# Optimization experiments

Measured on AMD Instinct MI355X. Metric: run time of the kernel, lower is better.

## Reference

```python
import jax, jax.numpy as jnp
import numpy as np

NUM_HEAD = 16


def setup_inputs() -> dict:
    key = jax.random.key(0)
    k1, k2, k3 = jax.random.split(key, 3)
    E = 1024
    x = jax.random.normal(k1, (4, 2048, E), dtype=jnp.float32)
    W1 = jax.random.normal(k2, (E, 3 * E), dtype=jnp.float32) * 0.02
    b1 = jnp.zeros((3 * E,), dtype=jnp.float32)
    W2 = jax.random.normal(k3, (E, E), dtype=jnp.float32) * 0.02
    b2 = jnp.zeros((E,), dtype=jnp.float32)
    return {"x": x, "W1": W1, "b1": b1, "W2": W2, "b2": b2}


def reference(x, W1, b1, W2, b2):
    # Fused QKV projection: (n, s, 3E)
    h = x @ W1 + b1
    n, s, _ = h.shape
    # Split into heads FIRST (matches torch reshape), then transpose: (n, H, s, 3*d_head)
    h = h.reshape(n, s, NUM_HEAD, -1).transpose(0, 2, 1, 3)
    # Chunk last dim into q, k, v: each (n, H, s, d_head)
    q, k, v = jnp.split(h, 3, axis=-1)
    dk = jnp.asarray(v.shape[-1], x.dtype) ** 0.5
    # Naive full S x S attention (faithful to source)
    w = jnp.einsum("nhqd,nhkd->nhqk", q, k) / dk
    w = jax.nn.softmax(w, axis=-1)  # dropout1 is identity at eval
    att = jnp.einsum("nhqk,nhkd->nhqd", w, v)
    att = att.transpose(0, 2, 1, 3).reshape(n, s, -1)  # (n, s, E)
    return att @ W2 + b2  # dropout2 identity at eval
```

## Files before the change

### kernel.cpp

```cpp
#include <hip/hip_runtime.h>
#include <math.h>
#include <stdint.h>
#include <stddef.h>


#define SEQ    2048
#define NB     4
#define E_DIM  1024
#define N1     3072
#define M_TOK  8192
#define NHEAD  16
#define DHEAD  64

typedef __attribute__((ext_vector_type(4))) float    floatx4;
typedef __attribute__((ext_vector_type(8))) short    shortx8;
typedef __attribute__((ext_vector_type(4))) short    shortx4;
typedef __attribute__((ext_vector_type(4))) unsigned short ushortx4;

#if __has_builtin(__builtin_amdgcn_exp2f)
#define EXP2(x) __builtin_amdgcn_exp2f(x)
#else
#define EXP2(x) __expf((x) * 0.6931471805599453f)
#endif

#define MFMA_K16(a, b, c) \
    __builtin_amdgcn_mfma_f32_16x16x16bf16_1k((a), (b), (c), 0, 0, 0)

__device__ __forceinline__ unsigned short f2bf(float f) {
    union { float f; unsigned u; } v; v.f = f;
    unsigned r = (v.u + 0x7FFFu + ((v.u >> 16) & 1u)) >> 16;
    return (unsigned short)r;
}
__device__ __forceinline__ unsigned fbits(float f) {
    union { float f; unsigned u; } v; v.f = f; return v.u;
}
__device__ __forceinline__ float bitsf(unsigned u) {
    union { unsigned u; float f; } v; v.u = u; return v.f;
}

__device__ __forceinline__ void gl_lds16(const void* g, void* l) {
    __builtin_amdgcn_global_load_lds(
        (const __attribute__((address_space(1))) unsigned int*)g,
        (__attribute__((address_space(3))) unsigned int*)l, 16, 0, 0);
}

__global__ __launch_bounds__(256) void cvt_bf16(
    const float* __restrict__ in, unsigned short* __restrict__ out)
{
    const size_t i = ((size_t)blockIdx.x * 256 + threadIdx.x) * 8;
    float4 a = *(const float4*)(in + i);
    float4 b = *(const float4*)(in + i + 4);
    ushortx4 o0 = { f2bf(a.x), f2bf(a.y), f2bf(a.z), f2bf(a.w) };
    ushortx4 o1 = { f2bf(b.x), f2bf(b.y), f2bf(b.z), f2bf(b.w) };
    *(ushortx4*)(out + i)     = o0;
    *(ushortx4*)(out + i + 4) = o1;
}

__global__ __launch_bounds__(256) void cvt_transpose(
    const float* __restrict__ W, unsigned short* __restrict__ Wt, int K, int N)
{
    __shared__ unsigned short tile[32][33];
    const int tx = threadIdx.x, ty = threadIdx.y;
    const int n0 = blockIdx.x * 32, k0 = blockIdx.y * 32;
#pragma unroll
    for (int r = 0; r < 4; ++r) {
        const int k = ty + r * 8;
        tile[tx][k] = f2bf(W[(size_t)(k0 + k) * N + n0 + tx]);
    }
    __syncthreads();
#pragma unroll
    for (int r = 0; r < 4; ++r) {
        const int n = ty + r * 8;
        Wt[(size_t)(n0 + n) * K + k0 + tx] = tile[n][tx];
    }
}

template <bool OUT_BF16, bool FUSE>
__global__ __launch_bounds__(256) void gemm_bf16(
    const short* __restrict__ A, const short* __restrict__ Bt,
    const float* __restrict__ bias, void* __restrict__ Cout,
    unsigned short* __restrict__ Vt,
    int M, int N, int K)
{
    __shared__ short As[2][128 * 64];
    __shared__ short Bs[2][128 * 64];

    const int t    = threadIdx.x;
    const int lane = t & 63, w = t >> 6;
    const int quad = lane >> 4, l15 = lane & 15;
    const int bm = blockIdx.y * 128, bn = blockIdx.x * 128;
    const int m0w = (w >> 1) * 64, n0w = (w & 1) * 64;

    const int srow   = t >> 3;
    const int schunk = t & 7;
    const int gch    = schunk ^ (srow & 7);
    const short* Ag = A  + (size_t)(bm + srow) * K + gch * 8;
    const short* Bg = Bt + (size_t)(bn + srow) * K + gch * 8;
    const int sOff = srow * 64 + schunk * 8;

    floatx4 acc[4][4];
#pragma unroll
    for (int i = 0; i < 4; ++i)
#pragma unroll
        for (int j = 0; j < 4; ++j) acc[i][j] = (floatx4)0.f;

    const int NK = K >> 6;

#define GEMM_STAGE(bufi, k0)                                                   \
    {                                                                          \
        _Pragma("unroll")                                                      \
        for (int r = 0; r < 4; ++r) {                                          \
            gl_lds16(Ag + (size_t)(r * 32) * K + (k0), &As[bufi][sOff + r * 32 * 64]); \
            gl_lds16(Bg + (size_t)(r * 32) * K + (k0), &Bs[bufi][sOff + r * 32 * 64]); \
        }                                                                      \
    }

    GEMM_STAGE(0, 0);
    GEMM_STAGE(1, 64);

    for (int kt = 0; kt < NK; ++kt) {
        const int buf = kt & 1;
        if (kt + 1 < NK) asm volatile("s_waitcnt vmcnt(8)" ::: "memory");
        else             asm volatile("s_waitcnt vmcnt(0)" ::: "memory");
        __builtin_amdgcn_sched_barrier(0);
        __builtin_amdgcn_s_barrier();
        __builtin_amdgcn_sched_barrier(0);

#pragma unroll
        for (int kk = 0; kk < 2; ++kk) {
            shortx8 af[4], bf[4];
#pragma unroll
            for (int mi = 0; mi < 4; ++mi)
                af[mi] = *(const shortx8*)(&As[buf][(m0w + mi * 16 + l15) * 64
                                           + (((kk * 4 + quad) ^ (l15 & 7)) * 8)]);
#pragma unroll
            for (int ni = 0; ni < 4; ++ni)
                bf[ni] = *(const shortx8*)(&Bs[buf][(n0w + ni * 16 + l15) * 64
                                           + (((kk * 4 + quad) ^ (l15 & 7)) * 8)]);
#pragma unroll
            for (int mi = 0; mi < 4; ++mi)
#pragma unroll
                for (int ni = 0; ni < 4; ++ni)
                    acc[mi][ni] = __builtin_amdgcn_mfma_f32_16x16x32_bf16(
                        af[mi], bf[ni], acc[mi][ni], 0, 0, 0);
        }

        __builtin_amdgcn_sched_barrier(0);
        __builtin_amdgcn_s_barrier();
        __builtin_amdgcn_sched_barrier(0);
        if (kt + 2 < NK) GEMM_STAGE(buf, (kt + 2) * 64);
    }
#undef GEMM_STAGE

    float bv[4];
#pragma unroll
    for (int ni = 0; ni < 4; ++ni) bv[ni] = bias[bn + n0w + ni * 16 + l15];

#pragma unroll
    for (int ni = 0; ni < 4; ++ni) {
        const int col   = bn + n0w + ni * 16 + l15;
        const int cm    = col % 192;
        const int vhead = col / 192;
#pragma unroll
        for (int mi = 0; mi < 4; ++mi) {
            const int row0 = bm + m0w + mi * 16 + quad * 4;
            float v[4];
#pragma unroll
            for (int r = 0; r < 4; ++r) v[r] = acc[mi][ni][r] + bv[ni];
            if (OUT_BF16) {
                if (FUSE && cm < DHEAD) {
#pragma unroll
                    for (int r = 0; r < 4; ++r) v[r] *= 0.18033688011112042f;
                }
                unsigned short* H = (unsigned short*)Cout;
#pragma unroll
                for (int r = 0; r < 4; ++r)
                    H[(size_t)(row0 + r) * N + col] = f2bf(v[r]);
                if (FUSE && cm >= 2 * DHEAD) {
                    const int nb = row0 >> 11;
                    const int s  = row0 & 2047;
                    const int d  = cm - 2 * DHEAD;
                    ushortx4 pk = { f2bf(v[0]), f2bf(v[1]), f2bf(v[2]), f2bf(v[3]) };
                    *(ushortx4*)(Vt + ((size_t)(nb * NHEAD + vhead) * DHEAD + d) * SEQ + s) = pk;
                }
            } else {
                float* C = (float*)Cout;
#pragma unroll
                for (int r = 0; r < 4; ++r)
                    C[(size_t)(row0 + r) * N + col] = v[r];
            }
        }
    }
}

__global__ __launch_bounds__(256, 4) void attn_mfma(
    const short* __restrict__ h, const short* __restrict__ Vt,
    unsigned short* __restrict__ att)
{
    __shared__ short Ks[2][64 * 64];
    __shared__ short Vs[2][64 * 64];

    const int t    = threadIdx.x;
    const int lane = t & 63, w = t >> 6;
    const int quad = lane >> 4, l15 = lane & 15;
    const int r7   = l15 & 7;
    const int bh = blockIdx.x, n = bh >> 4, head = bh & 15;
    const int q0 = blockIdx.y * 128 + w * 32;

    const short* hQ  = h + (size_t)n * SEQ * N1 + head * (3 * DHEAD);
    const short* hK  = hQ + DHEAD;
    const short* Vtb = Vt + (size_t)bh * DHEAD * SEQ;

    const int srow = t >> 2;
    const int sc0  = (t & 3) * 2;
    const int sk   = srow & 7;
    const short* gK = hK  + (size_t)srow * N1  + sc0 * 8;
    const short* gV = Vtb + (size_t)srow * SEQ + sc0 * 8;
    const int oL0 = srow * 64 + ((sc0    ) ^ sk) * 8;
    const int oL1 = srow * 64 + ((sc0 + 1) ^ sk) * 8;

    shortx8 qf[2][2];
#pragma unroll
    for (int qt = 0; qt < 2; ++qt)
#pragma unroll
        for (int kt = 0; kt < 2; ++kt)
            qf[qt][kt] = *(const shortx8*)(hQ + (size_t)(q0 + qt * 16 + l15) * N1
                                           + kt * 32 + quad * 8);

    floatx4 O[2][4];
    floatx4 Osum[2];
#pragma unroll
    for (int qt = 0; qt < 2; ++qt) {
        Osum[qt] = (floatx4)0.f;
#pragma unroll
        for (int dt = 0; dt < 4; ++dt) O[qt][dt] = (floatx4)0.f;
    }

    const shortx4 ones = { (short)0x3F80, (short)0x3F80, (short)0x3F80, (short)0x3F80 };

    const int NT = SEQ / 64;

    int4 ka = *(const int4*)gK, kb = *(const int4*)(gK + 8);
    int4 va = *(const int4*)gV, vb = *(const int4*)(gV + 8);
    *(int4*)(&Ks[0][oL0]) = ka; *(int4*)(&Ks[0][oL1]) = kb;
    *(int4*)(&Vs[0][oL0]) = va; *(int4*)(&Vs[0][oL1]) = vb;
    gK += (size_t)64 * N1; gV += 64;

    for (int it = 0; it < NT; ++it) {
        const int buf = it & 1;
        __syncthreads();

        const bool more = (it + 1 < NT);
        if (more) {
            ka = *(const int4*)gK; kb = *(const int4*)(gK + 8);
            va = *(const int4*)gV; vb = *(const int4*)(gV + 8);
            gK += (size_t)64 * N1; gV += 64;
        }

        const short* Kb = &Ks[buf][0];
        const short* Vb = &Vs[buf][0];

#pragma unroll
        for (int sl = 0; sl < 4; ++sl) {
            const short* krow = Kb + (sl * 16 + l15) * 64;
            shortx8 kf0 = *(const shortx8*)(krow + ((quad ^ r7) * 8));
            shortx8 kf1 = *(const shortx8*)(krow + (((quad ^ 4) ^ r7) * 8));
            shortx4 vf[4];
#pragma unroll
            for (int dt = 0; dt < 4; ++dt)
                vf[dt] = *(const shortx4*)(Vb + (dt * 16 + l15) * 64
                                           + (((sl * 4 + quad) ^ (r7 << 1)) << 2));

            shortx4 pa[2];
#pragma unroll
            for (int qt = 0; qt < 2; ++qt) {
                floatx4 s = __builtin_amdgcn_mfma_f32_16x16x32_bf16(
                    kf0, qf[qt][0], (floatx4)0.f, 0, 0, 0);
                s = __builtin_amdgcn_mfma_f32_16x16x32_bf16(
                    kf1, qf[qt][1], s, 0, 0, 0);
                const float p0 = EXP2(s[0]);
                const float p1 = EXP2(s[1]);
                const float p2 = EXP2(s[2]);
                const float p3 = EXP2(s[3]);
                union { uint2 u; shortx4 v; } cv;
                cv.u.x = __builtin_amdgcn_perm(fbits(p1), fbits(p0), 0x07060302u);
                cv.u.y = __builtin_amdgcn_perm(fbits(p3), fbits(p2), 0x07060302u);
                pa[qt] = cv.v;
            }

#pragma unroll
            for (int qt = 0; qt < 2; ++qt) {
                Osum[qt] = MFMA_K16(pa[qt], ones, Osum[qt]);
#pragma unroll
                for (int dt = 0; dt < 4; ++dt)
                    O[qt][dt] = MFMA_K16(pa[qt], vf[dt], O[qt][dt]);
            }
        }

        if (more) {
            short* Kn = &Ks[buf ^ 1][0];
            short* Vn = &Vs[buf ^ 1][0];
            *(int4*)(Kn + oL0) = ka; *(int4*)(Kn + oL1) = kb;
            *(int4*)(Vn + oL0) = va; *(int4*)(Vn + oL1) = vb;
        }
    }

    const size_t obase = ((size_t)n * SEQ + q0) * E_DIM + head * DHEAD;
#pragma unroll
    for (int qt = 0; qt < 2; ++qt)
#pragma unroll
        for (int r = 0; r < 4; ++r) {
            const float inv = 1.f / Osum[qt][r];
            const size_t row = obase + (size_t)(qt * 16 + quad * 4 + r) * E_DIM;
#pragma unroll
            for (int dt = 0; dt < 4; ++dt)
                att[row + dt * 16 + l15] = f2bf(O[qt][dt][r] * inv);
        }
}

extern "C" void kernel_launch(void* const* d_in, const int* in_sizes, int n_in,
                              void* d_out, int out_size, void* d_ws, size_t ws_size,
                              hipStream_t stream)
{
    const float* x  = (const float*)d_in[0];
    const float* W1 = (const float*)d_in[1];
    const float* b1 = (const float*)d_in[2];
    const float* W2 = (const float*)d_in[3];
    const float* b2 = (const float*)d_in[4];
    float* out = (float*)d_out;

    char* ws = (char*)d_ws;
    unsigned short* x_bf  = (unsigned short*)(ws);
    unsigned short* W1t   = (unsigned short*)(ws + (16u << 20));
    unsigned short* W2t   = (unsigned short*)(ws + (22u << 20));
    unsigned short* h_bf  = (unsigned short*)(ws + (24u << 20));
    unsigned short* attb  = (unsigned short*)(ws + (72u << 20));
    unsigned short* Vtw   = (unsigned short*)(ws + (88u << 20));

    cvt_bf16<<<dim3((M_TOK * E_DIM) / (256 * 8)), 256, 0, stream>>>(x, x_bf);
    cvt_transpose<<<dim3(N1 / 32, E_DIM / 32), dim3(32, 8), 0, stream>>>(W1, W1t, E_DIM, N1);
    cvt_transpose<<<dim3(E_DIM / 32, E_DIM / 32), dim3(32, 8), 0, stream>>>(W2, W2t, E_DIM, E_DIM);

    gemm_bf16<true, true><<<dim3(N1 / 128, M_TOK / 128), 256, 0, stream>>>(
        (const short*)x_bf, (const short*)W1t, b1, h_bf, Vtw, M_TOK, N1, E_DIM);

    attn_mfma<<<dim3(NB * NHEAD, SEQ / 128), 256, 0, stream>>>(
        (const short*)h_bf, (const short*)Vtw, attb);

    gemm_bf16<false, false><<<dim3(E_DIM / 128, M_TOK / 128), 256, 0, stream>>>(
        (const short*)attb, (const short*)W2t, b2, out, nullptr, M_TOK, E_DIM, E_DIM);
}
```

Before: 266.2 us.

## Rewrite attention inner loop with 32x32x16 MFMA and permlane32 P repacking

Replaces the 16x16 MFMA tiling of the attention kernel with 32x32x16 bf16 MFMAs, computing S^T per 32-key subtile and feeding P to the PV product after a permlane32_swap repack instead of a register round-trip. The row-sum of P is now accumulated with scalar adds and a cross-half shuffle, replacing the extra MFMA against a ones vector. It also raises wave priority around the compute section with s_setprio. The intent is fewer MFMA issues and less LDS fragment traffic per tile, at the cost of a new lane mapping that must be correct and possibly higher register pressure.

```diff
diff --git a/kernel.cpp b/kernel.cpp
--- a/kernel.cpp
+++ b/kernel.cpp
@@ -12,10 +12,11 @@
 #define NHEAD  16
 #define DHEAD  64
 
-typedef __attribute__((ext_vector_type(4))) float    floatx4;
-typedef __attribute__((ext_vector_type(8))) short    shortx8;
-typedef __attribute__((ext_vector_type(4))) short    shortx4;
-typedef __attribute__((ext_vector_type(4))) unsigned short ushortx4;
+typedef __attribute__((ext_vector_type(4)))  float    floatx4;
+typedef __attribute__((ext_vector_type(16))) float    floatx16;
+typedef __attribute__((ext_vector_type(8)))  short    shortx8;
+typedef __attribute__((ext_vector_type(4)))  short    shortx4;
+typedef __attribute__((ext_vector_type(4)))  unsigned short ushortx4;
 
 #if __has_builtin(__builtin_amdgcn_exp2f)
 #define EXP2(x) __builtin_amdgcn_exp2f(x)
@@ -23,8 +24,8 @@
 #define EXP2(x) __expf((x) * 0.6931471805599453f)
 #endif
 
-#define MFMA_K16(a, b, c) \
-    __builtin_amdgcn_mfma_f32_16x16x16bf16_1k((a), (b), (c), 0, 0, 0)
+#define MFMA32(a, b, c) \
+    __builtin_amdgcn_mfma_f32_32x32x16_bf16((a), (b), (c), 0, 0, 0)
 
 __device__ __forceinline__ unsigned short f2bf(float f) {
     union { float f; unsigned u; } v; v.f = f;
@@ -33,9 +34,6 @@
 }
 __device__ __forceinline__ unsigned fbits(float f) {
     union { float f; unsigned u; } v; v.f = f; return v.u;
-}
-__device__ __forceinline__ float bitsf(unsigned u) {
-    union { unsigned u; float f; } v; v.u = u; return v.f;
 }
 
 __device__ __forceinline__ void gl_lds16(const void* g, void* l) {
@@ -202,10 +200,9 @@
 
     const int t    = threadIdx.x;
     const int lane = t & 63, w = t >> 6;
-    const int quad = lane >> 4, l15 = lane & 15;
-    const int r7   = l15 & 7;
+    const int l31  = lane & 31, hf = lane >> 5;
     const int bh = blockIdx.x, n = bh >> 4, head = bh & 15;
-    const int q0 = blockIdx.y * 128 + w * 32;
+    const int q0w = blockIdx.y * 128 + w * 32;
 
     const short* hQ  = h + (size_t)n * SEQ * N1 + head * (3 * DHEAD);
     const short* hK  = hQ + DHEAD;
@@ -219,24 +216,14 @@
     const int oL0 = srow * 64 + ((sc0    ) ^ sk) * 8;
     const int oL1 = srow * 64 + ((sc0 + 1) ^ sk) * 8;
 
-    shortx8 qf[2][2];
-#pragma unroll
-    for (int qt = 0; qt < 2; ++qt)
-#pragma unroll
-        for (int kt = 0; kt < 2; ++kt)
-            qf[qt][kt] = *(const shortx8*)(hQ + (size_t)(q0 + qt * 16 + l15) * N1
-                                           + kt * 32 + quad * 8);
-
-    floatx4 O[2][4];
-    floatx4 Osum[2];
-#pragma unroll
-    for (int qt = 0; qt < 2; ++qt) {
-        Osum[qt] = (floatx4)0.f;
-#pragma unroll
-        for (int dt = 0; dt < 4; ++dt) O[qt][dt] = (floatx4)0.f;
-    }
-
-    const shortx4 ones = { (short)0x3F80, (short)0x3F80, (short)0x3F80, (short)0x3F80 };
+    shortx8 qf[4];
+#pragma unroll
+    for (int c = 0; c < 4; ++c)
+        qf[c] = *(const shortx8*)(hQ + (size_t)(q0w + l31) * N1 + c * 16 + hf * 8);
+
+    floatx16 O0 = (floatx16)0.f;
+    floatx16 O1 = (floatx16)0.f;
+    float ls0 = 0.f, ls1 = 0.f;
 
     const int NT = SEQ / 64;
 
@@ -260,42 +247,49 @@
         const short* Kb = &Ks[buf][0];
         const short* Vb = &Vs[buf][0];
 
-#pragma unroll
-        for (int sl = 0; sl < 4; ++sl) {
-            const short* krow = Kb + (sl * 16 + l15) * 64;
-            shortx8 kf0 = *(const shortx8*)(krow + ((quad ^ r7) * 8));
-            shortx8 kf1 = *(const shortx8*)(krow + (((quad ^ 4) ^ r7) * 8));
-            shortx4 vf[4];
-#pragma unroll
-            for (int dt = 0; dt < 4; ++dt)
-                vf[dt] = *(const shortx4*)(Vb + (dt * 16 + l15) * 64
-                                           + (((sl * 4 + quad) ^ (r7 << 1)) << 2));
-
-            shortx4 pa[2];
-#pragma unroll
-            for (int qt = 0; qt < 2; ++qt) {
-                floatx4 s = __builtin_amdgcn_mfma_f32_16x16x32_bf16(
-                    kf0, qf[qt][0], (floatx4)0.f, 0, 0, 0);
-                s = __builtin_amdgcn_mfma_f32_16x16x32_bf16(
-                    kf1, qf[qt][1], s, 0, 0, 0);
-                const float p0 = EXP2(s[0]);
-                const float p1 = EXP2(s[1]);
-                const float p2 = EXP2(s[2]);
-                const float p3 = EXP2(s[3]);
-                union { uint2 u; shortx4 v; } cv;
-                cv.u.x = __builtin_amdgcn_perm(fbits(p1), fbits(p0), 0x07060302u);
-                cv.u.y = __builtin_amdgcn_perm(fbits(p3), fbits(p2), 0x07060302u);
-                pa[qt] = cv.v;
+        __builtin_amdgcn_s_setprio(1);
+#pragma unroll
+        for (int sub = 0; sub < 2; ++sub) {
+            const int krow = sub * 32 + l31;
+            const short* kbase = Kb + krow * 64;
+            shortx8 kf[4];
+#pragma unroll
+            for (int c = 0; c < 4; ++c)
+                kf[c] = *(const shortx8*)(kbase + (((c * 2 + hf) ^ (krow & 7)) * 8));
+
+            floatx16 s = (floatx16)0.f;
+#pragma unroll
+            for (int c = 0; c < 4; ++c)
+                s = MFMA32(kf[c], qf[c], s);
+
+            float p[16];
+#pragma unroll
+            for (int i = 0; i < 8; ++i)  { p[i] = EXP2(s[i]); ls0 += p[i]; }
+#pragma unroll
+            for (int i = 8; i < 16; ++i) { p[i] = EXP2(s[i]); ls1 += p[i]; }
+
+#pragma unroll
+            for (int ks = 0; ks < 2; ++ks) {
+                const int b = ks * 8;
+                const unsigned A0 = __builtin_amdgcn_perm(fbits(p[b + 1]), fbits(p[b + 0]), 0x07060302u);
+                const unsigned A1 = __builtin_amdgcn_perm(fbits(p[b + 3]), fbits(p[b + 2]), 0x07060302u);
+                const unsigned B0 = __builtin_amdgcn_perm(fbits(p[b + 5]), fbits(p[b + 4]), 0x07060302u);
+                const unsigned B1 = __builtin_amdgcn_perm(fbits(p[b + 7]), fbits(p[b + 6]), 0x07060302u);
+                const auto r0 = __builtin_amdgcn_permlane32_swap(A0, B0, false, false);
+                const auto r1 = __builtin_amdgcn_permlane32_swap(A1, B1, false, false);
+                union { unsigned u[4]; shortx8 v; } pc;
+                pc.u[0] = r0[0]; pc.u[1] = r1[0]; pc.u[2] = r0[1]; pc.u[3] = r1[1];
+
+                const int vch = sub * 4 + ks * 2 + hf;
+                const int vr0 = l31;
+                const int vr1 = 32 + l31;
+                shortx8 vf0 = *(const shortx8*)(Vb + vr0 * 64 + ((vch ^ (vr0 & 7)) * 8));
+                shortx8 vf1 = *(const shortx8*)(Vb + vr1 * 64 + ((vch ^ (vr1 & 7)) * 8));
+                O0 = MFMA32(pc.v, vf0, O0);
+                O1 = MFMA32(pc.v, vf1, O1);
             }
-
-#pragma unroll
-            for (int qt = 0; qt < 2; ++qt) {
-                Osum[qt] = MFMA_K16(pa[qt], ones, Osum[qt]);
-#pragma unroll
-                for (int dt = 0; dt < 4; ++dt)
-                    O[qt][dt] = MFMA_K16(pa[qt], vf[dt], O[qt][dt]);
-            }
-        }
+        }
+        __builtin_amdgcn_s_setprio(0);
 
         if (more) {
             short* Kn = &Ks[buf ^ 1][0];
@@ -305,17 +299,18 @@
         }
     }
 
-    const size_t obase = ((size_t)n * SEQ + q0) * E_DIM + head * DHEAD;
-#pragma unroll
-    for (int qt = 0; qt < 2; ++qt)
-#pragma unroll
-        for (int r = 0; r < 4; ++r) {
-            const float inv = 1.f / Osum[qt][r];
-            const size_t row = obase + (size_t)(qt * 16 + quad * 4 + r) * E_DIM;
-#pragma unroll
-            for (int dt = 0; dt < 4; ++dt)
-                att[row + dt * 16 + l15] = f2bf(O[qt][dt][r] * inv);
-        }
+    float tot = ls0 + ls1;
+    tot += __shfl_xor(tot, 32);
+
+    const size_t obase = ((size_t)n * SEQ + q0w) * E_DIM + head * DHEAD;
+#pragma unroll
+    for (int reg = 0; reg < 16; ++reg) {
+        const int qr = (reg & 3) + 8 * (reg >> 2) + 4 * hf;
+        const float inv = 1.f / __shfl(tot, qr);
+        const size_t row = obase + (size_t)qr * E_DIM;
+        att[row + l31]      = f2bf(O0[reg] * inv);
+        att[row + 32 + l31] = f2bf(O1[reg] * inv);
+    }
 }
 
 extern "C" void kernel_launch(void* const* d_in, const int* in_sizes, int n_in,
```

New measurement: 295.0 us. 10.8% more time.
